# Performance work log

Hardware: AMD Instinct MI355X
Metric: run time of the kernel (lower is better)

## Reference

```python
import jax, jax.numpy as jnp
import numpy as np
import math

N_EMBD = 1024
N_HEAD = 16
HEAD_DIM = N_EMBD // N_HEAD
B, T = 2, 2048
LORA_RANK = 16      # 8-bit setting
LORA_SCALE = 32.0 / 16.0  # alpha / rank
QMIN, QMAX = 0.0, 255.0   # 8-bit asymmetric


def round_ste(x):
    return x + jax.lax.stop_gradient(jnp.round(x) - x)


def fake_quant(x, scale, zero_point):
    # LearnableFakeQuantize, asymmetric 8-bit, straight-through round
    q = jnp.clip(round_ste(x / scale + zero_point), QMIN, QMAX)
    return (q - zero_point) * scale


def lora_linear(x, w, b, la, lb):
    # base linear + LoRA path (dropout disabled / eval)
    return x @ w + b + LORA_SCALE * ((x @ la) @ lb)


def setup_inputs() -> dict:
    key = jax.random.key(0)
    ks = jax.random.split(key, 10)
    std = 0.02
    hidden_states = jax.random.normal(ks[0], (B, T, N_EMBD), dtype=jnp.float32)
    w_attn = jax.random.normal(ks[1], (N_EMBD, 3 * N_EMBD), dtype=jnp.float32) * std
    b_attn = jnp.zeros((3 * N_EMBD,), dtype=jnp.float32)
    la_attn = jax.random.normal(ks[2], (N_EMBD, LORA_RANK), dtype=jnp.float32) * std
    lb_attn = jnp.zeros((LORA_RANK, 3 * N_EMBD), dtype=jnp.float32)
    w_proj = jax.random.normal(ks[3], (N_EMBD, N_EMBD), dtype=jnp.float32) * std
    b_proj = jnp.zeros((N_EMBD,), dtype=jnp.float32)
    la_proj = jax.random.normal(ks[4], (N_EMBD, LORA_RANK), dtype=jnp.float32) * std
    lb_proj = jnp.zeros((LORA_RANK, N_EMBD), dtype=jnp.float32)
    kv_scale = jnp.asarray(0.05, dtype=jnp.float32)
    kv_zero_point = jnp.asarray(128.0, dtype=jnp.float32)
    return {
        'hidden_states': hidden_states,
        'w_attn': w_attn, 'b_attn': b_attn, 'la_attn': la_attn, 'lb_attn': lb_attn,
        'w_proj': w_proj, 'b_proj': b_proj, 'la_proj': la_proj, 'lb_proj': lb_proj,
        'kv_scale': kv_scale, 'kv_zero_point': kv_zero_point,
    }


def reference(hidden_states, w_attn, b_attn, la_attn, lb_attn,
              w_proj, b_proj, la_proj, lb_proj, kv_scale, kv_zero_point):
    Bn, Tn, C = hidden_states.shape
    qkv = lora_linear(hidden_states, w_attn, b_attn, la_attn, lb_attn)
    q, k, v = jnp.split(qkv, 3, axis=2)
    # [B, T, C] -> [B, H, T, D]
    def to_heads(x):
        return x.reshape(Bn, Tn, N_HEAD, HEAD_DIM).transpose(0, 2, 1, 3)
    q, k, v = to_heads(q), to_heads(k), to_heads(v)
    k = fake_quant(k, kv_scale, kv_zero_point)
    v = fake_quant(v, kv_scale, kv_zero_point)
    scores = jnp.einsum('bhqd,bhkd->bhqk', q, k) / math.sqrt(HEAD_DIM)
    causal = jnp.tril(jnp.ones((Tn, Tn), dtype=bool))
    scores = jnp.where(causal, scores, -jnp.inf)
    attn = jax.nn.softmax(scores, axis=-1)
    out = jnp.einsum('bhqk,bhkd->bhqd', attn, v)
    out = out.transpose(0, 2, 1, 3).reshape(Bn, Tn, C)
    return lora_linear(out, w_proj, b_proj, la_proj, lb_proj)
```

## Files before the change

### kernel.cpp

```cpp
#include <hip/hip_runtime.h>
#include <hip/hip_bf16.h>
#include <math.h>

#define N_EMBD   1024
#define N_HEAD   16
#define HEAD_DIM 64
#define BATCH    2
#define TSEQ     2048
#define RANK     16
#define LORA_SCALE 2.0f
#define M_TOTAL  (BATCH * TSEQ)
#define C3       (3 * N_EMBD)

typedef unsigned short ushort_t;
typedef __attribute__((ext_vector_type(8))) short bf16x8;
typedef __attribute__((ext_vector_type(4))) float f32x4;

__device__ __forceinline__ float fake_quant(float x, float scale, float zp) {
    float q = rintf(x / scale + zp);
    q = fminf(fmaxf(q, 0.0f), 255.0f);
    return (q - zp) * scale;
}

__device__ __forceinline__ ushort_t bf16bits(float f) {
    union { __hip_bfloat16 h; ushort_t u; } c;
    c.h = __float2bfloat16(f);
    return c.u;
}

__device__ __forceinline__ float bfraw2f(ushort_t u) {
    union { unsigned int i; float f; } c; c.i = ((unsigned int)u) << 16; return c.f;
}

#define NB_LORA 1024
#define NB_TRA  3072
#define NB_TRP  1024
#define NB_CVT  4096

__device__ __forceinline__ void transpose_body(
        const float* __restrict__ in, __hip_bfloat16* __restrict__ hiT,
        __hip_bfloat16* __restrict__ loT, int R, int C,
        int c0, int r0, int tid, float* sh) {
    float (*tl)[33] = (float(*)[33])sh;
    const int tx = tid & 31, ty = tid >> 5;
    for (int i = ty; i < 32; i += 8)
        tl[i][tx] = in[(size_t)(r0 + i) * C + c0 + tx];
    __syncthreads();
    for (int i = ty; i < 32; i += 8) {
        float v = tl[tx][i];
        __hip_bfloat16 h = __float2bfloat16(v);
        size_t o = (size_t)(c0 + i) * R + r0 + tx;
        hiT[o] = h;
        if (loT) loT[o] = __float2bfloat16(v - __bfloat162float(h));
    }
}

__global__ __launch_bounds__(256)
void prep_kernel(const float* __restrict__ x,
                 const float* __restrict__ w_attn,
                 const float* __restrict__ w_proj,
                 const float* __restrict__ la_attn,
                 __hip_bfloat16* __restrict__ x_hi,
                 __hip_bfloat16* __restrict__ x_lo,
                 __hip_bfloat16* __restrict__ wqT_h,
                 __hip_bfloat16* __restrict__ wqT_l,
                 __hip_bfloat16* __restrict__ wpT,
                 float* __restrict__ t_attn_p) {
    __shared__ float sh[33 * 32];
    const int tid = threadIdx.x;
    int b = blockIdx.x;

    if (b < NB_LORA) {
        const int bx = b & 255, by = b >> 8;
        float (*Xs)[64] = (float(*)[64])sh;
        const int ty = tid >> 4, tx = tid & 15;
        const int row0 = bx * 16;
        const int kbase = by * 256;
        float acc = 0.0f;
        for (int k0 = kbase; k0 < kbase + 256; k0 += 64) {
            int rr = tid >> 4, kk = (tid & 15) * 4;
            float4 v = *(const float4*)(x + (size_t)(row0 + rr) * N_EMBD + k0 + kk);
            Xs[rr][kk] = v.x; Xs[rr][kk + 1] = v.y; Xs[rr][kk + 2] = v.z; Xs[rr][kk + 3] = v.w;
            __syncthreads();
            for (int k = 0; k < 64; ++k)
                acc += Xs[ty][k] * la_attn[(size_t)(k0 + k) * RANK + tx];
            __syncthreads();
        }
        t_attn_p[((size_t)by * M_TOTAL + row0 + ty) * RANK + tx] = acc;
        return;
    }
    b -= NB_LORA;
    if (b < NB_TRA) {
        const int gx = b % (C3 / 32), gy = b / (C3 / 32);
        transpose_body(w_attn, wqT_h, wqT_l, N_EMBD, C3, gx * 32, gy * 32, tid, sh);
        return;
    }
    b -= NB_TRA;
    if (b < NB_TRP) {
        const int gx = b & 31, gy = b >> 5;
        transpose_body(w_proj, wpT, nullptr, N_EMBD, N_EMBD, gx * 32, gy * 32, tid, sh);
        return;
    }
    b -= NB_TRP;
    {
        const int i = b * 256 + tid;
        float4 v = ((const float4*)x)[i];
        float vs[4] = {v.x, v.y, v.z, v.w};
        #pragma unroll
        for (int k = 0; k < 4; ++k) {
            __hip_bfloat16 h = __float2bfloat16(vs[k]);
            x_hi[i * 4 + k] = h;
            x_lo[i * 4 + k] = __float2bfloat16(vs[k] - __bfloat162float(h));
        }
    }
}

__global__ void vtrans_kernel(const ushort_t* __restrict__ Vb,
                              ushort_t* __restrict__ Vt) {
    __shared__ ushort_t tl[64][68];
    const int bh = blockIdx.x & 31, tt = blockIdx.x >> 5;
    const int tid = threadIdx.x;
    {
        const int t = tid >> 2, d0 = (tid & 3) * 16;
        const uint4 u = *(const uint4*)(Vb + ((size_t)bh * TSEQ + tt * 64 + t) * 64 + d0);
        *(uint4*)&tl[t][d0] = u;
        *(uint4*)&tl[t][d0 + 8] = *(const uint4*)(Vb + ((size_t)bh * TSEQ + tt * 64 + t) * 64 + d0 + 8);
    }
    __syncthreads();
    const int d = tid >> 2, t0 = (tid & 3) * 16;
    unsigned int wbuf[8];
    #pragma unroll
    for (int j = 0; j < 8; ++j)
        wbuf[j] = (unsigned int)tl[t0 + 2 * j][d] | ((unsigned int)tl[t0 + 2 * j + 1][d] << 16);
    ushort_t* dst = Vt + ((size_t)bh * 64 + d) * TSEQ + tt * 64 + t0;
    *(uint4*)dst       = make_uint4(wbuf[0], wbuf[1], wbuf[2], wbuf[3]);
    *(uint4*)(dst + 8) = make_uint4(wbuf[4], wbuf[5], wbuf[6], wbuf[7]);
}

__global__ void lora_t_part_bf16_kernel(const ushort_t* __restrict__ x,
                                        const float* __restrict__ la,
                                        float* __restrict__ tpart, int K) {
    __shared__ float Xs[16][64];
    const int tid = threadIdx.x;
    const int ty = tid >> 4, tx = tid & 15;
    const int row0 = blockIdx.x * 16;
    const int kbase = blockIdx.y * 256;
    float acc = 0.0f;
    for (int k0 = kbase; k0 < kbase + 256; k0 += 64) {
        int rr = tid >> 4, kk = (tid & 15) * 4;
        const ushort4 u = *(const ushort4*)(x + (size_t)(row0 + rr) * K + k0 + kk);
        Xs[rr][kk] = bfraw2f(u.x); Xs[rr][kk + 1] = bfraw2f(u.y);
        Xs[rr][kk + 2] = bfraw2f(u.z); Xs[rr][kk + 3] = bfraw2f(u.w);
        __syncthreads();
        for (int k = 0; k < 64; ++k)
            acc += Xs[ty][k] * la[(size_t)(k0 + k) * RANK + tx];
        __syncthreads();
    }
    tpart[((size_t)blockIdx.y * M_TOTAL + row0 + ty) * RANK + tx] = acc;
}

__device__ __forceinline__ int sw_off(int r, int c) {
    return ((r >> 1) << 7) + (((((r & 1) << 2) | c) ^ ((r >> 1) & 7)) << 4);
}

template <bool SPLIT>
__global__ __launch_bounds__(256, 3)
void gemm_mfma_kernel(const __hip_bfloat16* __restrict__ Ah,
                      const __hip_bfloat16* __restrict__ Al,
                      const __hip_bfloat16* __restrict__ Bh,
                      const __hip_bfloat16* __restrict__ Bl,
                      const float* __restrict__ bias,
                      const float* __restrict__ tpart,
                      const float* __restrict__ lb,
                      float* __restrict__ Cf,
                      ushort_t* __restrict__ Qb,
                      ushort_t* __restrict__ Kb,
                      ushort_t* __restrict__ Vb,
                      const float* __restrict__ sp,
                      const float* __restrict__ zp,
                      int M, int N, int K, int split_col0, int out_mode) {
    constexpr int TILE = 128 * 32;
    __shared__ __align__(16) __hip_bfloat16 As[3 * TILE];
    __shared__ __align__(16) __hip_bfloat16 Bs[3 * TILE];
    float* Ts = (float*)As;
    float* Ls = (float*)Bs;

    const int tid = threadIdx.x;
    const int lane = tid & 63, w = tid >> 6;

    int bcol, brow;
    {
        const int NC = gridDim.x, NR = gridDim.y;
        const int lid = blockIdx.y * NC + blockIdx.x;
        const int xcd = lid & 7, s = lid >> 3;
        const int cw = NC >> 1, rh = NR >> 2;
        const int cg = xcd & 1, rg = xcd >> 1;
        if (SPLIT) {
            bcol = 2 * (s % cw) + cg;
            brow = rg * rh + (s / cw);
        } else {
            bcol = cg * cw + (s % cw);
            brow = rg * rh + (s / cw);
        }
    }
    const int row0 = brow * 128, col0 = bcol * 128;
    const int wr = (w >> 1) * 64, wc = (w & 1) * 64;
    const bool do_split = SPLIT && (col0 >= split_col0);

    const int s_lc = (lane & 7) ^ ((lane >> 3) & 7);
    const int s_rb = 2 * (lane >> 3) + (s_lc >> 2);
    const int s_c8 = (s_lc & 3) * 8;

    float qsc = 0.f, qzp = 0.f;
    if (out_mode == 1) { qsc = sp[0]; qzp = zp[0]; }

    f32x4 acc[4][4];
    #pragma unroll
    for (int i = 0; i < 4; ++i)
        #pragma unroll
        for (int j = 0; j < 4; ++j)
            acc[i][j] = (f32x4){0.f, 0.f, 0.f, 0.f};

    const int arow = wr + (lane & 15);
    const int chunk = lane >> 4;

    const ushort_t* alp[4];
    const ushort_t* blp[4];
    if (do_split) {
        #pragma unroll
        for (int mi = 0; mi < 4; ++mi)
            alp[mi] = (const ushort_t*)Al + (size_t)(row0 + arow + mi * 16) * K + chunk * 8;
        #pragma unroll
        for (int nj = 0; nj < 4; ++nj)
            blp[nj] = (const ushort_t*)Bl + (size_t)(col0 + wc + nj * 16 + (lane & 15)) * K + chunk * 8;
    }

    auto stage = [&](int buf, int kidx) {
        const int k0 = kidx << 5;
        __hip_bfloat16* dA = As + buf * TILE;
        __hip_bfloat16* dB = Bs + buf * TILE;
        #pragma unroll
        for (int qq = 0; qq < 2; ++qq) {
            const int q = 2 * w + qq;
            const int r = 16 * q + s_rb;
            const __hip_bfloat16* gA = Ah + (size_t)(row0 + r) * K + k0 + s_c8;
            __builtin_amdgcn_global_load_lds(
                (const __attribute__((address_space(1))) void*)gA,
                (__attribute__((address_space(3))) void*)(dA + q * 512), 16, 0, 0);
            const __hip_bfloat16* gB = Bh + (size_t)(col0 + r) * K + k0 + s_c8;
            __builtin_amdgcn_global_load_lds(
                (const __attribute__((address_space(1))) void*)gB,
                (__attribute__((address_space(3))) void*)(dB + q * 512), 16, 0, 0);
        }
    };

    const int KI = K >> 5;
    stage(0, 0);
    stage(1, 1);
    int bcur = 0, bstage = 2;
    for (int kk = 0; kk < KI; ++kk) {
        if (kk == KI - 1) {
            asm volatile("s_waitcnt vmcnt(0)" ::: "memory");
        } else {
            asm volatile("s_waitcnt vmcnt(4)" ::: "memory");
        }
        __builtin_amdgcn_s_barrier();

        const int k0 = kk << 5;
        bf16x8 a_l[4], b_l[4];
        if (do_split) {
            #pragma unroll
            for (int mi = 0; mi < 4; ++mi) a_l[mi] = *(const bf16x8*)(alp[mi] + k0);
            #pragma unroll
            for (int nj = 0; nj < 4; ++nj) b_l[nj] = *(const bf16x8*)(blp[nj] + k0);
        }
        if (kk + 2 < KI) { stage(bstage, kk + 2); bstage = (bstage == 2) ? 0 : bstage + 1; }

        const char* ab = (const char*)(As + bcur * TILE);
        const char* bb = (const char*)(Bs + bcur * TILE);
        bf16x8 a_h[4], b_h[4];
        #pragma unroll
        for (int mi = 0; mi < 4; ++mi)
            a_h[mi] = *(const bf16x8*)(ab + sw_off(arow + mi * 16, chunk));
        #pragma unroll
        for (int nj = 0; nj < 4; ++nj)
            b_h[nj] = *(const bf16x8*)(bb + sw_off(wc + nj * 16 + (lane & 15), chunk));
        #pragma unroll
        for (int mi = 0; mi < 4; ++mi)
            #pragma unroll
            for (int nj = 0; nj < 4; ++nj)
                acc[mi][nj] = __builtin_amdgcn_mfma_f32_16x16x32_bf16(a_h[mi], b_h[nj], acc[mi][nj], 0, 0, 0);
        if (do_split) {
            #pragma unroll
            for (int mi = 0; mi < 4; ++mi)
                #pragma unroll
                for (int nj = 0; nj < 4; ++nj) {
                    acc[mi][nj] = __builtin_amdgcn_mfma_f32_16x16x32_bf16(a_h[mi], b_l[nj], acc[mi][nj], 0, 0, 0);
                    acc[mi][nj] = __builtin_amdgcn_mfma_f32_16x16x32_bf16(a_l[mi], b_h[nj], acc[mi][nj], 0, 0, 0);
                }
        }
        bcur = (bcur == 2) ? 0 : bcur + 1;
    }
    __syncthreads();

    {
        int r = tid >> 1, j0 = (tid & 1) * 8;
        float4 t0 = {0, 0, 0, 0}, t1 = {0, 0, 0, 0};
        #pragma unroll
        for (int c = 0; c < 4; ++c) {
            const float* src = tpart + ((size_t)c * M_TOTAL + row0 + r) * RANK + j0;
            float4 s0 = *(const float4*)src;
            float4 s1 = *(const float4*)(src + 4);
            t0.x += s0.x; t0.y += s0.y; t0.z += s0.z; t0.w += s0.w;
            t1.x += s1.x; t1.y += s1.y; t1.z += s1.z; t1.w += s1.w;
        }
        *(float4*)(Ts + r * 16 + j0)     = t0;
        *(float4*)(Ts + r * 16 + j0 + 4) = t1;
        int rr = tid >> 4, c0 = (tid & 15) * 8;
        const float4* lsrc = (const float4*)(lb + (size_t)rr * N + col0 + c0);
        float4* ldst = (float4*)(Ls + rr * 128 + c0);
        ldst[0] = lsrc[0]; ldst[1] = lsrc[1];
    }
    __syncthreads();
    #pragma unroll
    for (int mi = 0; mi < 4; ++mi)
        #pragma unroll
        for (int nj = 0; nj < 4; ++nj) {
            const int coll = wc + nj * 16 + (lane & 15);
            const float bv = bias[col0 + coll];
            #pragma unroll
            for (int rg = 0; rg < 4; ++rg) {
                const int rowl = wr + mi * 16 + (lane >> 4) * 4 + rg;
                float lsum = 0.f;
                #pragma unroll
                for (int rr = 0; rr < 16; ++rr)
                    lsum += Ts[rowl * 16 + rr] * Ls[rr * 128 + coll];
                const float val = acc[mi][nj][rg] + bv + LORA_SCALE * lsum;
                if (out_mode == 0) {
                    Cf[(size_t)(row0 + rowl) * N + col0 + coll] = val;
                } else {
                    const int R = row0 + rowl;
                    const int b = R >> 11, t = R & 2047;
                    const int CN = col0 + coll;
                    const int sec = CN >> 10, head = (CN >> 6) & 15, d = CN & 63;
                    const size_t off = (((size_t)(b * 16 + head)) * TSEQ + t) * 64 + d;
                    if (sec == 0)      Qb[off] = bf16bits(val * 0.125f);
                    else if (sec == 1) Kb[off] = bf16bits(fake_quant(val, qsc, qzp));
                    else               Vb[off] = bf16bits(fake_quant(val, qsc, qzp));
                }
            }
        }
}

__global__ __launch_bounds__(256)
void mfma_attn_kernel(const ushort_t* __restrict__ Qb,
                      const ushort_t* __restrict__ Kq,
                      const ushort_t* __restrict__ Vtq,
                      ushort_t* __restrict__ outb) {
    const int bx = blockIdx.x;
    const int bh = bx & 31;
    const int qt = 31 - (bx >> 5);
    const int b = bh >> 4, h = bh & 15;
    const int tid = threadIdx.x;
    const int lane = tid & 63, w = tid >> 6;
    const int m16 = lane & 15, qc = lane >> 4;
    const int m7 = m16 & 7;

    __shared__ ushort_t Qs[4096];
    __shared__ ushort_t Ks[2][4096];
    __shared__ ushort_t Vs[2][4096];
    __shared__ ushort_t Ps[4096];

    const int s_g = (lane & 7) ^ ((lane >> 3) & 7);
    const int s_r = lane >> 3;

    const ushort_t* Qg = Qb + (size_t)bh * TSEQ * 64;
    const ushort_t* Kg = Kq + (size_t)bh * TSEQ * 64;
    const ushort_t* Vg = Vtq + (size_t)bh * 64 * TSEQ;

    auto stageKV = [&](int buf, int kt) {
        #pragma unroll
        for (int pp = 0; pp < 2; ++pp) {
            const int p = 2 * w + pp;
            const ushort_t* gk = Kg + ((size_t)(kt * 64 + 8 * p + s_r)) * 64 + s_g * 8;
            __builtin_amdgcn_global_load_lds(
                (const __attribute__((address_space(1))) void*)gk,
                (__attribute__((address_space(3))) void*)(Ks[buf] + p * 512), 16, 0, 0);
            const ushort_t* gv = Vg + ((size_t)(8 * p + s_r)) * TSEQ + kt * 64 + s_g * 8;
            __builtin_amdgcn_global_load_lds(
                (const __attribute__((address_space(1))) void*)gv,
                (__attribute__((address_space(3))) void*)(Vs[buf] + p * 512), 16, 0, 0);
        }
    };

    #pragma unroll
    for (int pp = 0; pp < 2; ++pp) {
        const int p = 2 * w + pp;
        const ushort_t* gq = Qg + ((size_t)(qt * 64 + 8 * p + s_r)) * 64 + s_g * 8;
        __builtin_amdgcn_global_load_lds(
            (const __attribute__((address_space(1))) void*)gq,
            (__attribute__((address_space(3))) void*)(Qs + p * 512), 16, 0, 0);
    }
    stageKV(0, 0);
    __syncthreads();

    bf16x8 a_q[2];
    {
        const int row = 16 * w + m16;
        #pragma unroll
        for (int c = 0; c < 2; ++c) {
            const int g = qc + 4 * c;
            a_q[c] = *(const bf16x8*)((const char*)Qs + row * 128 + ((g ^ m7) << 4));
        }
    }

    float m_st[4], l_st[4];
    f32x4 o_acc[4];
    #pragma unroll
    for (int r = 0; r < 4; ++r) { m_st[r] = -INFINITY; l_st[r] = 0.0f; }
    #pragma unroll
    for (int dj = 0; dj < 4; ++dj) o_acc[dj] = (f32x4){0.f, 0.f, 0.f, 0.f};

    for (int kt = 0; kt <= qt; ++kt) {
        const int cur = kt & 1;
        if (kt < qt) stageKV(cur ^ 1, kt + 1);

        const bool diag = (kt == qt);
        const int nj_hi = diag ? (w + 1) : 4;

        f32x4 s[4];
        #pragma unroll
        for (int nj = 0; nj < 4; ++nj) s[nj] = (f32x4){0.f, 0.f, 0.f, 0.f};
        #pragma unroll
        for (int c = 0; c < 2; ++c) {
            #pragma unroll
            for (int nj = 0; nj < 4; ++nj) {
                if (nj < nj_hi) {
                    const int row = 16 * nj + m16;
                    const int g = qc + 4 * c;
                    bf16x8 bk = *(const bf16x8*)((const char*)Ks[cur] + row * 128 + ((g ^ m7) << 4));
                    s[nj] = __builtin_amdgcn_mfma_f32_16x16x32_bf16(a_q[c], bk, s[nj], 0, 0, 0);
                }
            }
        }

        float alpha[4], p_[4][4];
        #pragma unroll
        for (int reg = 0; reg < 4; ++reg) {
            const int qrow = 16 * w + 4 * qc + reg;
            float sv[4];
            float rm = -INFINITY;
            #pragma unroll
            for (int nj = 0; nj < 4; ++nj) {
                float v = s[nj][reg];
                if (diag && (m16 + 16 * nj > qrow)) v = -INFINITY;
                sv[nj] = v;
                rm = fmaxf(rm, v);
            }
            #pragma unroll
            for (int off = 1; off < 16; off <<= 1)
                rm = fmaxf(rm, __shfl_xor(rm, off, 16));
            const float mo = m_st[reg];
            const float mn = fmaxf(mo, rm);
            const float al = __expf(mo - mn);
            float rs = 0.f;
            #pragma unroll
            for (int nj = 0; nj < 4; ++nj) {
                float pv = __expf(sv[nj] - mn);
                p_[reg][nj] = pv;
                rs += pv;
            }
            #pragma unroll
            for (int off = 1; off < 16; off <<= 1)
                rs += __shfl_xor(rs, off, 16);
            l_st[reg] = al * l_st[reg] + rs;
            m_st[reg] = mn;
            alpha[reg] = al;
        }

        #pragma unroll
        for (int reg = 0; reg < 4; ++reg) {
            const int row = 16 * w + 4 * qc + reg;
            const int r7 = row & 7;
            #pragma unroll
            for (int nj = 0; nj < 4; ++nj) {
                const int k = m16 + 16 * nj;
                Ps[row * 64 + (((k >> 3) ^ r7) << 3) + (k & 7)] = bf16bits(p_[reg][nj]);
            }
        }

        #pragma unroll
        for (int dj = 0; dj < 4; ++dj)
            #pragma unroll
            for (int reg = 0; reg < 4; ++reg)
                o_acc[dj][reg] *= alpha[reg];

        const int c_hi = diag ? (w >= 2 ? 2 : 1) : 2;
        #pragma unroll
        for (int c = 0; c < 2; ++c) {
            if (c < c_hi) {
                const int rowp = 16 * w + m16;
                const int g = qc + 4 * c;
                bf16x8 ap = *(const bf16x8*)((const char*)Ps + rowp * 128 + ((g ^ m7) << 4));
                #pragma unroll
                for (int dj = 0; dj < 4; ++dj) {
                    const int rowv = 16 * dj + m16;
                    bf16x8 bv = *(const bf16x8*)((const char*)Vs[cur] + rowv * 128 + ((g ^ m7) << 4));
                    o_acc[dj] = __builtin_amdgcn_mfma_f32_16x16x32_bf16(ap, bv, o_acc[dj], 0, 0, 0);
                }
            }
        }
        __syncthreads();
    }

    #pragma unroll
    for (int reg = 0; reg < 4; ++reg) {
        const float inv = 1.0f / l_st[reg];
        const int q = qt * 64 + 16 * w + 4 * qc + reg;
        #pragma unroll
        for (int dj = 0; dj < 4; ++dj) {
            const int d = m16 + 16 * dj;
            outb[((size_t)b * TSEQ + q) * N_EMBD + h * 64 + d] = bf16bits(o_acc[dj][reg] * inv);
        }
    }
}

extern "C" void kernel_launch(void* const* d_in, const int* in_sizes, int n_in,
                              void* d_out, int out_size, void* d_ws, size_t ws_size,
                              hipStream_t stream) {
    const float* x        = (const float*)d_in[0];
    const float* w_attn   = (const float*)d_in[1];
    const float* b_attn   = (const float*)d_in[2];
    const float* la_attn  = (const float*)d_in[3];
    const float* lb_attn  = (const float*)d_in[4];
    const float* w_proj   = (const float*)d_in[5];
    const float* b_proj   = (const float*)d_in[6];
    const float* la_proj  = (const float*)d_in[7];
    const float* lb_proj  = (const float*)d_in[8];
    const float* kv_scale = (const float*)d_in[9];
    const float* kv_zp    = (const float*)d_in[10];
    float* out = (float*)d_out;

    char* ws = (char*)d_ws;
    float* t_attn_p       = (float*)ws;          ws += (size_t)4 * M_TOTAL * RANK * 4;
    float* t_proj_p       = (float*)ws;          ws += (size_t)4 * M_TOTAL * RANK * 4;
    ushort_t* aob         = (ushort_t*)ws;       ws += (size_t)M_TOTAL * N_EMBD * 2;
    __hip_bfloat16* x_hi  = (__hip_bfloat16*)ws; ws += (size_t)M_TOTAL * N_EMBD * 2;
    __hip_bfloat16* x_lo  = (__hip_bfloat16*)ws; ws += (size_t)M_TOTAL * N_EMBD * 2;
    __hip_bfloat16* wqT_h = (__hip_bfloat16*)ws; ws += (size_t)C3 * N_EMBD * 2;
    __hip_bfloat16* wqT_l = (__hip_bfloat16*)ws; ws += (size_t)C3 * N_EMBD * 2;
    __hip_bfloat16* wpT   = (__hip_bfloat16*)ws; ws += (size_t)N_EMBD * N_EMBD * 2;
    ushort_t* Qb          = (ushort_t*)ws;       ws += (size_t)32 * TSEQ * 64 * 2;
    ushort_t* Kb          = (ushort_t*)ws;       ws += (size_t)32 * TSEQ * 64 * 2;
    ushort_t* Vb          = (ushort_t*)ws;       ws += (size_t)32 * TSEQ * 64 * 2;
    ushort_t* Vtq         = (ushort_t*)ws;       ws += (size_t)32 * 64 * TSEQ * 2;

    prep_kernel<<<dim3(NB_LORA + NB_TRA + NB_TRP + NB_CVT), 256, 0, stream>>>(
        x, w_attn, w_proj, la_attn,
        x_hi, x_lo, wqT_h, wqT_l, wpT, t_attn_p);

    gemm_mfma_kernel<true><<<dim3(24, 32), 256, 0, stream>>>(
        x_hi, x_lo, wqT_h, wqT_l, b_attn, t_attn_p, lb_attn,
        nullptr, Qb, Kb, Vb, kv_scale, kv_zp,
        M_TOTAL, C3, N_EMBD, 2 * N_EMBD, 1);

    vtrans_kernel<<<dim3(32 * (TSEQ / 64)), 256, 0, stream>>>(Vb, Vtq);

    mfma_attn_kernel<<<dim3(32 * 32), 256, 0, stream>>>(Qb, Kb, Vtq, aob);

    lora_t_part_bf16_kernel<<<dim3(M_TOTAL / 16, 4), 256, 0, stream>>>(aob, la_proj, t_proj_p, N_EMBD);

    gemm_mfma_kernel<false><<<dim3(8, 32), 256, 0, stream>>>(
        (const __hip_bfloat16*)aob, nullptr, wpT, nullptr, b_proj, t_proj_p, lb_proj,
        out, nullptr, nullptr, nullptr, nullptr, nullptr,
        M_TOTAL, N_EMBD, N_EMBD, 1 << 30, 0);
}
```

Baseline: 309.1 us.

## Use 64-row tiles for output projection GEMM and tighten attention KV barriers

Templates the GEMM kernel on the M tile height and launches the output projection with 64x128 tiles on a doubled grid. The goal is to fill more of the GPU's compute units on that small GEMM, which had only 256 blocks. The attention loop now waits on the async KV loads with an explicit vmcnt and s_barrier instead of relying on __syncthreads. The smaller tiles reduce reuse of B per block, and the hand-written waits depend on the exact count of outstanding loads being correct.

```diff
diff --git a/kernel.cpp b/kernel.cpp
--- a/kernel.cpp
+++ b/kernel.cpp
@@ -163,7 +163,7 @@
     return ((r >> 1) << 7) + (((((r & 1) << 2) | c) ^ ((r >> 1) & 7)) << 4);
 }
 
-template <bool SPLIT>
+template <bool SPLIT, int TM>
 __global__ __launch_bounds__(256, 3)
 void gemm_mfma_kernel(const __hip_bfloat16* __restrict__ Ah,
                       const __hip_bfloat16* __restrict__ Al,
@@ -179,9 +179,11 @@
                       const float* __restrict__ sp,
                       const float* __restrict__ zp,
                       int M, int N, int K, int split_col0, int out_mode) {
-    constexpr int TILE = 128 * 32;
-    __shared__ __align__(16) __hip_bfloat16 As[3 * TILE];
-    __shared__ __align__(16) __hip_bfloat16 Bs[3 * TILE];
+    constexpr int TILEA = TM * 32;
+    constexpr int TILEB = 128 * 32;
+    constexpr int MI = TM / 32;
+    __shared__ __align__(16) __hip_bfloat16 As[3 * TILEA];
+    __shared__ __align__(16) __hip_bfloat16 Bs[3 * TILEB];
     float* Ts = (float*)As;
     float* Ls = (float*)Bs;
 
@@ -203,8 +205,8 @@
             brow = rg * rh + (s / cw);
         }
     }
-    const int row0 = brow * 128, col0 = bcol * 128;
-    const int wr = (w >> 1) * 64, wc = (w & 1) * 64;
+    const int row0 = brow * TM, col0 = bcol * 128;
+    const int wr = (w >> 1) * (TM >> 1), wc = (w & 1) * 64;
     const bool do_split = SPLIT && (col0 >= split_col0);
 
     const int s_lc = (lane & 7) ^ ((lane >> 3) & 7);
@@ -214,9 +216,9 @@
     float qsc = 0.f, qzp = 0.f;
     if (out_mode == 1) { qsc = sp[0]; qzp = zp[0]; }
 
-    f32x4 acc[4][4];
+    f32x4 acc[MI][4];
     #pragma unroll
-    for (int i = 0; i < 4; ++i)
+    for (int i = 0; i < MI; ++i)
         #pragma unroll
         for (int j = 0; j < 4; ++j)
             acc[i][j] = (f32x4){0.f, 0.f, 0.f, 0.f};
@@ -228,7 +230,7 @@
     const ushort_t* blp[4];
     if (do_split) {
         #pragma unroll
-        for (int mi = 0; mi < 4; ++mi)
+        for (int mi = 0; mi < MI; ++mi)
             alp[mi] = (const ushort_t*)Al + (size_t)(row0 + arow + mi * 16) * K + chunk * 8;
         #pragma unroll
         for (int nj = 0; nj < 4; ++nj)
@@ -237,20 +239,37 @@
 
     auto stage = [&](int buf, int kidx) {
         const int k0 = kidx << 5;
-        __hip_bfloat16* dA = As + buf * TILE;
-        __hip_bfloat16* dB = Bs + buf * TILE;
-        #pragma unroll
-        for (int qq = 0; qq < 2; ++qq) {
-            const int q = 2 * w + qq;
-            const int r = 16 * q + s_rb;
-            const __hip_bfloat16* gA = Ah + (size_t)(row0 + r) * K + k0 + s_c8;
+        __hip_bfloat16* dA = As + buf * TILEA;
+        __hip_bfloat16* dB = Bs + buf * TILEB;
+        if (TM == 128) {
+            #pragma unroll
+            for (int qq = 0; qq < 2; ++qq) {
+                const int q = 2 * w + qq;
+                const int r = 16 * q + s_rb;
+                const __hip_bfloat16* gA = Ah + (size_t)(row0 + r) * K + k0 + s_c8;
+                __builtin_amdgcn_global_load_lds(
+                    (const __attribute__((address_space(1))) void*)gA,
+                    (__attribute__((address_space(3))) void*)(dA + q * 512), 16, 0, 0);
+                const __hip_bfloat16* gB = Bh + (size_t)(col0 + r) * K + k0 + s_c8;
+                __builtin_amdgcn_global_load_lds(
+                    (const __attribute__((address_space(1))) void*)gB,
+                    (__attribute__((address_space(3))) void*)(dB + q * 512), 16, 0, 0);
+            }
+        } else {
+            const int rA = 16 * w + s_rb;
+            const __hip_bfloat16* gA = Ah + (size_t)(row0 + rA) * K + k0 + s_c8;
             __builtin_amdgcn_global_load_lds(
                 (const __attribute__((address_space(1))) void*)gA,
-                (__attribute__((address_space(3))) void*)(dA + q * 512), 16, 0, 0);
-            const __hip_bfloat16* gB = Bh + (size_t)(col0 + r) * K + k0 + s_c8;
-            __builtin_amdgcn_global_load_lds(
-                (const __attribute__((address_space(1))) void*)gB,
-                (__attribute__((address_space(3))) void*)(dB + q * 512), 16, 0, 0);
+                (__attribute__((address_space(3))) void*)(dA + w * 512), 16, 0, 0);
+            #pragma unroll
+            for (int qq = 0; qq < 2; ++qq) {
+                const int q = 2 * w + qq;
+                const int r = 16 * q + s_rb;
+                const __hip_bfloat16* gB = Bh + (size_t)(col0 + r) * K + k0 + s_c8;
+                __builtin_amdgcn_global_load_lds(
+                    (const __attribute__((address_space(1))) void*)gB,
+                    (__attribute__((address_space(3))) void*)(dB + q * 512), 16, 0, 0);
+            }
         }
     };
 
@@ -261,38 +280,40 @@
     for (int kk = 0; kk < KI; ++kk) {
         if (kk == KI - 1) {
             asm volatile("s_waitcnt vmcnt(0)" ::: "memory");
+        } else if (TM == 128) {
+            asm volatile("s_waitcnt vmcnt(4)" ::: "memory");
         } else {
-            asm volatile("s_waitcnt vmcnt(4)" ::: "memory");
+            asm volatile("s_waitcnt vmcnt(3)" ::: "memory");
         }
         __builtin_amdgcn_s_barrier();
 
         const int k0 = kk << 5;
-        bf16x8 a_l[4], b_l[4];
+        bf16x8 a_l[MI], b_l[4];
         if (do_split) {
             #pragma unroll
-            for (int mi = 0; mi < 4; ++mi) a_l[mi] = *(const bf16x8*)(alp[mi] + k0);
+            for (int mi = 0; mi < MI; ++mi) a_l[mi] = *(const bf16x8*)(alp[mi] + k0);
             #pragma unroll
             for (int nj = 0; nj < 4; ++nj) b_l[nj] = *(const bf16x8*)(blp[nj] + k0);
         }
         if (kk + 2 < KI) { stage(bstage, kk + 2); bstage = (bstage == 2) ? 0 : bstage + 1; }
 
-        const char* ab = (const char*)(As + bcur * TILE);
-        const char* bb = (const char*)(Bs + bcur * TILE);
-        bf16x8 a_h[4], b_h[4];
-        #pragma unroll
-        for (int mi = 0; mi < 4; ++mi)
+        const char* ab = (const char*)(As + bcur * TILEA);
+        const char* bb = (const char*)(Bs + bcur * TILEB);
+        bf16x8 a_h[MI], b_h[4];
+        #pragma unroll
+        for (int mi = 0; mi < MI; ++mi)
             a_h[mi] = *(const bf16x8*)(ab + sw_off(arow + mi * 16, chunk));
         #pragma unroll
         for (int nj = 0; nj < 4; ++nj)
             b_h[nj] = *(const bf16x8*)(bb + sw_off(wc + nj * 16 + (lane & 15), chunk));
         #pragma unroll
-        for (int mi = 0; mi < 4; ++mi)
+        for (int mi = 0; mi < MI; ++mi)
             #pragma unroll
             for (int nj = 0; nj < 4; ++nj)
                 acc[mi][nj] = __builtin_amdgcn_mfma_f32_16x16x32_bf16(a_h[mi], b_h[nj], acc[mi][nj], 0, 0, 0);
         if (do_split) {
             #pragma unroll
-            for (int mi = 0; mi < 4; ++mi)
+            for (int mi = 0; mi < MI; ++mi)
                 #pragma unroll
                 for (int nj = 0; nj < 4; ++nj) {
                     acc[mi][nj] = __builtin_amdgcn_mfma_f32_16x16x32_bf16(a_h[mi], b_l[nj], acc[mi][nj], 0, 0, 0);
@@ -305,17 +326,19 @@
 
     {
         int r = tid >> 1, j0 = (tid & 1) * 8;
-        float4 t0 = {0, 0, 0, 0}, t1 = {0, 0, 0, 0};
-        #pragma unroll
-        for (int c = 0; c < 4; ++c) {
-            const float* src = tpart + ((size_t)c * M_TOTAL + row0 + r) * RANK + j0;
-            float4 s0 = *(const float4*)src;
-            float4 s1 = *(const float4*)(src + 4);
-            t0.x += s0.x; t0.y += s0.y; t0.z += s0.z; t0.w += s0.w;
-            t1.x += s1.x; t1.y += s1.y; t1.z += s1.z; t1.w += s1.w;
-        }
-        *(float4*)(Ts + r * 16 + j0)     = t0;
-        *(float4*)(Ts + r * 16 + j0 + 4) = t1;
+        if (r < TM) {
+            float4 t0 = {0, 0, 0, 0}, t1 = {0, 0, 0, 0};
+            #pragma unroll
+            for (int c = 0; c < 4; ++c) {
+                const float* src = tpart + ((size_t)c * M_TOTAL + row0 + r) * RANK + j0;
+                float4 s0 = *(const float4*)src;
+                float4 s1 = *(const float4*)(src + 4);
+                t0.x += s0.x; t0.y += s0.y; t0.z += s0.z; t0.w += s0.w;
+                t1.x += s1.x; t1.y += s1.y; t1.z += s1.z; t1.w += s1.w;
+            }
+            *(float4*)(Ts + r * 16 + j0)     = t0;
+            *(float4*)(Ts + r * 16 + j0 + 4) = t1;
+        }
         int rr = tid >> 4, c0 = (tid & 15) * 8;
         const float4* lsrc = (const float4*)(lb + (size_t)rr * N + col0 + c0);
         float4* ldst = (float4*)(Ls + rr * 128 + c0);
@@ -323,7 +346,7 @@
     }
     __syncthreads();
     #pragma unroll
-    for (int mi = 0; mi < 4; ++mi)
+    for (int mi = 0; mi < MI; ++mi)
         #pragma unroll
         for (int nj = 0; nj < 4; ++nj) {
             const int coll = wc + nj * 16 + (lane & 15);
@@ -423,7 +446,13 @@
 
     for (int kt = 0; kt <= qt; ++kt) {
         const int cur = kt & 1;
-        if (kt < qt) stageKV(cur ^ 1, kt + 1);
+        if (kt < qt) {
+            stageKV(cur ^ 1, kt + 1);
+            asm volatile("s_waitcnt vmcnt(4)" ::: "memory");
+        } else {
+            asm volatile("s_waitcnt vmcnt(0)" ::: "memory");
+        }
+        __builtin_amdgcn_s_barrier();
 
         const bool diag = (kt == qt);
         const int nj_hi = diag ? (w + 1) : 4;
@@ -510,7 +539,7 @@
                 }
             }
         }
-        __syncthreads();
+        asm volatile("s_barrier" ::: "memory");
     }
 
     #pragma unroll
@@ -559,7 +588,7 @@
         x, w_attn, w_proj, la_attn,
         x_hi, x_lo, wqT_h, wqT_l, wpT, t_attn_p);
 
-    gemm_mfma_kernel<true><<<dim3(24, 32), 256, 0, stream>>>(
+    gemm_mfma_kernel<true, 128><<<dim3(24, 32), 256, 0, stream>>>(
         x_hi, x_lo, wqT_h, wqT_l, b_attn, t_attn_p, lb_attn,
         nullptr, Qb, Kb, Vb, kv_scale, kv_zp,
         M_TOTAL, C3, N_EMBD, 2 * N_EMBD, 1);
@@ -570,7 +599,7 @@
 
     lora_t_part_bf16_kernel<<<dim3(M_TOTAL / 16, 4), 256, 0, stream>>>(aob, la_proj, t_proj_p, N_EMBD);
 
-    gemm_mfma_kernel<false><<<dim3(8, 32), 256, 0, stream>>>(
+    gemm_mfma_kernel<false, 64><<<dim3(8, 64), 256, 0, stream>>>(
         (const __hip_bfloat16*)aob, nullptr, wpT, nullptr, b_proj, t_proj_p, lb_proj,
         out, nullptr, nullptr, nullptr, nullptr, nullptr,
         M_TOTAL, N_EMBD, N_EMBD, 1 << 30, 0);
```

New measurement: 297.0 us. -3.9%, faster.
